# Kernel optimization log

Hardware: AMD Instinct MI355X
Metric: run time of the kernel (lower is better)

Reference implementation:

```python
import jax, jax.numpy as jnp
import numpy as np

N_SAMPLES, N_TIME, N_FEAT = 64, 4, 64
N_ENTITIES = 10000
D = N_TIME * N_FEAT  # 256
K = 10


def setup_inputs() -> dict:
    key = jax.random.key(0)
    k1, k2 = jax.random.split(key)
    query = jax.random.uniform(k1, (N_SAMPLES, N_TIME, N_FEAT), dtype=jnp.float32)
    # module state: self.enity_info, flattened view must be [n_entities, D]
    enity_info = jax.random.uniform(k2, (N_ENTITIES, D), dtype=jnp.float32)
    return {"query": query, "enity_info": enity_info, "k": K}


def reference(query, enity_info, k):
    n_samples = query.shape[0]
    q = query.reshape(n_samples, -1)                 # [n, d]
    e = enity_info.reshape(enity_info.shape[0], -1)  # [m, d]
    # pairwise Jaccard: sum(min) / sum(max) over feature dim
    inter = jnp.sum(jnp.minimum(q[:, None, :], e[None, :, :]), axis=2)  # [n, m]
    union = jnp.sum(jnp.maximum(q[:, None, :], e[None, :, :]), axis=2)  # [n, m]
    jaccard = inter / union                                             # [n, m]
    # torch.topk largest=True, sorted=True -> lax.top_k (descending)
    _, top_idx = jax.lax.top_k(jaccard, k)
    # torch.topk largest=False, sorted=True -> ascending smallest: top_k of negated
    _, bot_idx = jax.lax.top_k(-jaccard, k)
    return top_idx, bot_idx
```

## Files before the change

kernel.cpp:

```cpp
#include <hip/hip_runtime.h>
#include <math.h>
#include <limits.h>

#define NQ     64
#define NE     10000
#define K      10
#define NBLK   500
#define EPB    20
#define TPB    256
#define NWAVE  4
#define EPW    5
#define SLOT   11
#define SCALE  8388608.0f

__device__ __forceinline__ bool better_top(double v, int i, double v2, int i2) {
    return (v > v2) || (v == v2 && i < i2);
}

__device__ __forceinline__ void merge_slots16(double* Mv, unsigned short* Mi, int A, int B) {
    double ov[K]; unsigned short oi[K];
    int a = 0, b = 0;
#pragma unroll
    for (int o = 0; o < K; ++o) {
        double va = Mv[A * SLOT + a]; int ia = Mi[A * SLOT + a];
        double vb = Mv[B * SLOT + b]; int ib = Mi[B * SLOT + b];
        bool pick = better_top(va, ia, vb, ib);
        ov[o] = pick ? va : vb;
        oi[o] = (unsigned short)(pick ? ia : ib);
        if (pick) ++a; else ++b;
    }
#pragma unroll
    for (int o = 0; o < K; ++o) { Mv[A * SLOT + o] = ov[o]; Mi[A * SLOT + o] = oi[o]; }
}

#define CSWAP(v, ii, A, B)                                                 \
    {                                                                      \
        bool c_ = better_top(v[B], ii[B], v[A], ii[A]);                    \
        double tv_ = c_ ? v[B] : v[A]; double uv_ = c_ ? v[A] : v[B];      \
        int    ti_ = c_ ? ii[B] : ii[A]; int ui_ = c_ ? ii[A] : ii[B];     \
        v[A] = tv_; v[B] = uv_; ii[A] = ti_; ii[B] = ui_;                  \
    }
#define SORT5(v, ii)            \
    CSWAP(v, ii, 0, 1) CSWAP(v, ii, 3, 4) CSWAP(v, ii, 2, 4) \
    CSWAP(v, ii, 2, 3) CSWAP(v, ii, 0, 3) CSWAP(v, ii, 0, 2) \
    CSWAP(v, ii, 1, 4) CSWAP(v, ii, 1, 3) CSWAP(v, ii, 1, 2)

__global__ __launch_bounds__(256) void ent_sums(const float* __restrict__ E,
                                                unsigned* __restrict__ Se) {
    const int w = threadIdx.x >> 6, l = threadIdx.x & 63;
    const int j = blockIdx.x * 4 + w;
    float4 v = reinterpret_cast<const float4*>(E)[(size_t)j * 64 + l];
    unsigned s = (unsigned)(v.x * SCALE) + (unsigned)(v.y * SCALE)
               + (unsigned)(v.z * SCALE) + (unsigned)(v.w * SCALE);
#pragma unroll
    for (int m = 1; m < 64; m <<= 1) s += (unsigned)__shfl_xor((int)s, m, 64);
    if (l == 0) Se[j] = s;
}

__global__ __launch_bounds__(TPB, 2) void jac_part(
        const float* __restrict__ Q, const float* __restrict__ E,
        const unsigned* __restrict__ Se,
        double* __restrict__ pvT, double* __restrict__ pvB,
        int* __restrict__ piT, int* __restrict__ piB) {
    __shared__ uint4 QT[64 * 65];

    const int t = threadIdx.x;
    const int l = t & 63;
    const int w = t >> 6;
    const int b = blockIdx.x;
    const int ebase = b * EPB + w * EPW;

    const float4* E4 = (const float4*)E;
    const float4* Q4 = (const float4*)Q;

    float4 er[EPW];
#pragma unroll
    for (int s = 0; s < EPW; ++s) er[s] = E4[(size_t)(ebase + s) * 64 + l];
    unsigned se[EPW];
#pragma unroll
    for (int s = 0; s < EPW; ++s) se[s] = Se[ebase + s];

#pragma unroll
    for (int it = 0; it < 16; ++it) {
        const int f = t + TPB * it;
        float4 v = Q4[f];
        uint4 u;
        u.x = (unsigned)(v.x * SCALE); u.y = (unsigned)(v.y * SCALE);
        u.z = (unsigned)(v.z * SCALE); u.w = (unsigned)(v.w * SCALE);
        QT[(f & 63) * 65 + (f >> 6)] = u;
    }

    uint4 eu[EPW];
#pragma unroll
    for (int s = 0; s < EPW; ++s) {
        eu[s].x = (unsigned)(er[s].x * SCALE); eu[s].y = (unsigned)(er[s].y * SCALE);
        eu[s].z = (unsigned)(er[s].z * SCALE); eu[s].w = (unsigned)(er[s].w * SCALE);
    }
    __syncthreads();

    unsigned a0[EPW], a1[EPW];
#pragma unroll
    for (int s = 0; s < EPW; ++s) { a0[s] = 0; a1[s] = 0; }
    unsigned sq = 0;

#pragma unroll 8
    for (int g = 0; g < 64; ++g) {
        uint4 qv = QT[g * 65 + l];
        sq += (qv.x + qv.y) + (qv.z + qv.w);
#pragma unroll
        for (int s = 0; s < EPW; ++s) {
            unsigned ex = (unsigned)__builtin_amdgcn_readlane((int)eu[s].x, g);
            unsigned ey = (unsigned)__builtin_amdgcn_readlane((int)eu[s].y, g);
            unsigned ez = (unsigned)__builtin_amdgcn_readlane((int)eu[s].z, g);
            unsigned ew = (unsigned)__builtin_amdgcn_readlane((int)eu[s].w, g);
            a0[s] += min(qv.x, ex) + min(qv.y, ey);
            a1[s] += min(qv.z, ez) + min(qv.w, ew);
        }
    }

    double av[EPW]; int ai[EPW]; double bv[EPW]; int bi[EPW];
#pragma unroll
    for (int s = 0; s < EPW; ++s) {
        unsigned inter = a0[s] + a1[s];
        unsigned uni   = sq + se[s] - inter;
        double jac = (double)inter / (double)uni;
        av[s] = jac;  ai[s] = ebase + s;
        bv[s] = -jac; bi[s] = ebase + s;
    }
    SORT5(av, ai)
    SORT5(bv, bi)

    __syncthreads();
    double*         MvA = (double*)&QT[0];
    unsigned short* MiA = (unsigned short*)((char*)&QT[0] + 22528);
    double*         MvB = (double*)((char*)&QT[0] + 28160);
    unsigned short* MiB = (unsigned short*)((char*)&QT[0] + 50688);
    const int slot = w * 64 + l;

#pragma unroll
    for (int o = 0; o < EPW; ++o) {
        MvA[slot * SLOT + o] = av[o]; MiA[slot * SLOT + o] = (unsigned short)ai[o];
        MvB[slot * SLOT + o] = bv[o]; MiB[slot * SLOT + o] = (unsigned short)bi[o];
    }
#pragma unroll
    for (int o = EPW; o < K; ++o) {
        MvA[slot * SLOT + o] = -INFINITY; MiA[slot * SLOT + o] = 0xFFFFu;
        MvB[slot * SLOT + o] = -INFINITY; MiB[slot * SLOT + o] = 0xFFFFu;
    }
    __syncthreads();

    if (w < 2) {
        merge_slots16(MvA, MiA, w * 64 + l, (w + 2) * 64 + l);
        merge_slots16(MvB, MiB, w * 64 + l, (w + 2) * 64 + l);
    }
    __syncthreads();
    if (w == 0) {
        merge_slots16(MvA, MiA, l, 64 + l);
        merge_slots16(MvB, MiB, l, 64 + l);
        const size_t off = ((size_t)l * NBLK + b) * K;
#pragma unroll
        for (int o = 0; o < K; ++o) {
            pvT[off + o] = MvA[l * SLOT + o]; piT[off + o] = (int)MiA[l * SLOT + o];
            pvB[off + o] = MvB[l * SLOT + o]; piB[off + o] = (int)MiB[l * SLOT + o];
        }
    }
}

__global__ __launch_bounds__(256) void final_extract(
        const double* __restrict__ pvT, const double* __restrict__ pvB,
        const int* __restrict__ piT, const int* __restrict__ piB,
        int* __restrict__ out) {
    __shared__ double Lv[256 * K];
    __shared__ int    Li[256 * K];
    __shared__ double Wv[4];
    __shared__ int    Wi[4], Wo[4];
    __shared__ int    res[K];

    const int bid = blockIdx.x;
    const int q   = bid >> 1;
    const bool top = (bid & 1) == 0;
    const int t   = threadIdx.x;
    const int l   = t & 63;
    const int w   = t >> 6;

    const double* V = (top ? pvT : pvB) + (size_t)q * NBLK * K;
    const int*    I = (top ? piT : piB) + (size_t)q * NBLK * K;

    {
        double ov[K]; int oi[K];
        const int lb = t + 256;
        if (lb < NBLK) {
            int a = 0, bn = 0;
            const size_t sa = (size_t)t * K, sb = (size_t)lb * K;
#pragma unroll
            for (int o = 0; o < K; ++o) {
                double va = V[sa + a];  int ia = I[sa + a];
                double vb = V[sb + bn]; int ib = I[sb + bn];
                bool pick = better_top(va, ia, vb, ib);
                ov[o] = pick ? va : vb; oi[o] = pick ? ia : ib;
                if (pick) ++a; else ++bn;
            }
        } else {
#pragma unroll
            for (int o = 0; o < K; ++o) { ov[o] = V[(size_t)t * K + o]; oi[o] = I[(size_t)t * K + o]; }
        }
#pragma unroll
        for (int o = 0; o < K; ++o) { Lv[t * K + o] = ov[o]; Li[t * K + o] = oi[o]; }
    }
    __syncthreads();

    int h = 0;
    double hv = Lv[t * K];
    int    hi = Li[t * K];

    for (int r = 0; r < K; ++r) {
        double v = hv; int idx = hi; int own = t;
#pragma unroll
        for (int m = 1; m < 64; m <<= 1) {
            double ov = __shfl_xor(v, m, 64);
            int    oi = __shfl_xor(idx, m, 64);
            int    oo = __shfl_xor(own, m, 64);
            if (better_top(ov, oi, v, idx)) { v = ov; idx = oi; own = oo; }
        }
        if (l == 0) { Wv[w] = v; Wi[w] = idx; Wo[w] = own; }
        __syncthreads();
        double gv = Wv[0]; int gi = Wi[0], go = Wo[0];
#pragma unroll
        for (int ww = 1; ww < 4; ++ww)
            if (better_top(Wv[ww], Wi[ww], gv, gi)) { gv = Wv[ww]; gi = Wi[ww]; go = Wo[ww]; }
        if (t == go) {
            ++h;
            bool ok = h < K;
            hv = ok ? Lv[t * K + h] : -INFINITY;
            hi = ok ? Li[t * K + h] : INT_MAX;
        }
        if (t == 0) res[r] = gi;
        __syncthreads();
    }

    if (t < K) out[(top ? 0 : NQ * K) + q * K + t] = res[t];
}

extern "C" void kernel_launch(void* const* d_in, const int* in_sizes, int n_in,
                              void* d_out, int out_size, void* d_ws, size_t ws_size,
                              hipStream_t stream) {
    const float* Q = (const float*)d_in[0];
    const float* E = (const float*)d_in[1];
    int* out = (int*)d_out;

    char* ws = (char*)d_ws;
    unsigned* Se  = (unsigned*)(ws);
    double*   pvT = (double*)(ws + 40960);
    double*   pvB = (double*)(ws + 2600960);
    int*      piT = (int*)   (ws + 5160960);
    int*      piB = (int*)   (ws + 6440960);

    hipLaunchKernelGGL(ent_sums, dim3(NE / 4), dim3(256), 0, stream, E, Se);
    hipLaunchKernelGGL(jac_part, dim3(NBLK), dim3(TPB), 0, stream,
                       Q, E, Se, pvT, pvB, piT, piB);
    hipLaunchKernelGGL(final_extract, dim3(NQ * 2), dim3(256), 0, stream,
                       pvT, pvB, piT, piB, out);
}
```

Measured before the change: 53.33 us.

## Use 512-thread blocks with two entities per wave and 16-bit partial indices

```diff
diff --git a/kernel.cpp b/kernel.cpp
--- a/kernel.cpp
+++ b/kernel.cpp
@@ -5,11 +5,10 @@
 #define NQ     64
 #define NE     10000
 #define K      10
-#define NBLK   500
-#define EPB    20
-#define TPB    256
-#define NWAVE  4
-#define EPW    5
+#define NBLK   625
+#define EPB    16
+#define TPB    512
+#define EPW    2
 #define SLOT   11
 #define SCALE  8388608.0f
 
@@ -33,6 +32,25 @@
     for (int o = 0; o < K; ++o) { Mv[A * SLOT + o] = ov[o]; Mi[A * SLOT + o] = oi[o]; }
 }
 
+__device__ __forceinline__ void merge_lds_global(double* Lv, int* Li, int slot,
+                                                 const double* __restrict__ V,
+                                                 const unsigned short* __restrict__ I,
+                                                 int src) {
+    double ov[K]; int oi[K];
+    int a = 0, b = 0;
+#pragma unroll
+    for (int o = 0; o < K; ++o) {
+        double va = Lv[slot * K + a]; int ia = Li[slot * K + a];
+        double vb = V[(size_t)src * K + b]; int ib = (int)I[(size_t)src * K + b];
+        bool pick = better_top(va, ia, vb, ib);
+        ov[o] = pick ? va : vb;
+        oi[o] = pick ? ia : ib;
+        if (pick) ++a; else ++b;
+    }
+#pragma unroll
+    for (int o = 0; o < K; ++o) { Lv[slot * K + o] = ov[o]; Li[slot * K + o] = oi[o]; }
+}
+
 #define CSWAP(v, ii, A, B)                                                 \
     {                                                                      \
         bool c_ = better_top(v[B], ii[B], v[A], ii[A]);                    \
@@ -40,10 +58,6 @@
         int    ti_ = c_ ? ii[B] : ii[A]; int ui_ = c_ ? ii[A] : ii[B];     \
         v[A] = tv_; v[B] = uv_; ii[A] = ti_; ii[B] = ui_;                  \
     }
-#define SORT5(v, ii)            \
-    CSWAP(v, ii, 0, 1) CSWAP(v, ii, 3, 4) CSWAP(v, ii, 2, 4) \
-    CSWAP(v, ii, 2, 3) CSWAP(v, ii, 0, 3) CSWAP(v, ii, 0, 2) \
-    CSWAP(v, ii, 1, 4) CSWAP(v, ii, 1, 3) CSWAP(v, ii, 1, 2)
 
 __global__ __launch_bounds__(256) void ent_sums(const float* __restrict__ E,
                                                 unsigned* __restrict__ Se) {
@@ -61,7 +75,7 @@
         const float* __restrict__ Q, const float* __restrict__ E,
         const unsigned* __restrict__ Se,
         double* __restrict__ pvT, double* __restrict__ pvB,
-        int* __restrict__ piT, int* __restrict__ piB) {
+        unsigned short* __restrict__ piT, unsigned short* __restrict__ piB) {
     __shared__ uint4 QT[64 * 65];
 
     const int t = threadIdx.x;
@@ -81,7 +95,7 @@
     for (int s = 0; s < EPW; ++s) se[s] = Se[ebase + s];
 
 #pragma unroll
-    for (int it = 0; it < 16; ++it) {
+    for (int it = 0; it < 8; ++it) {
         const int f = t + TPB * it;
         float4 v = Q4[f];
         uint4 u;
@@ -127,48 +141,49 @@
         av[s] = jac;  ai[s] = ebase + s;
         bv[s] = -jac; bi[s] = ebase + s;
     }
-    SORT5(av, ai)
-    SORT5(bv, bi)
-
-    __syncthreads();
-    double*         MvA = (double*)&QT[0];
-    unsigned short* MiA = (unsigned short*)((char*)&QT[0] + 22528);
-    double*         MvB = (double*)((char*)&QT[0] + 28160);
-    unsigned short* MiB = (unsigned short*)((char*)&QT[0] + 50688);
+    CSWAP(av, ai, 0, 1)
+    CSWAP(bv, bi, 0, 1)
+
+    __syncthreads();
+    double*         Mv = (double*)&QT[0];
+    unsigned short* Mi = (unsigned short*)((char*)&QT[0] + 45056);
     const int slot = w * 64 + l;
 
 #pragma unroll
-    for (int o = 0; o < EPW; ++o) {
-        MvA[slot * SLOT + o] = av[o]; MiA[slot * SLOT + o] = (unsigned short)ai[o];
-        MvB[slot * SLOT + o] = bv[o]; MiB[slot * SLOT + o] = (unsigned short)bi[o];
-    }
-#pragma unroll
-    for (int o = EPW; o < K; ++o) {
-        MvA[slot * SLOT + o] = -INFINITY; MiA[slot * SLOT + o] = 0xFFFFu;
-        MvB[slot * SLOT + o] = -INFINITY; MiB[slot * SLOT + o] = 0xFFFFu;
-    }
-    __syncthreads();
-
-    if (w < 2) {
-        merge_slots16(MvA, MiA, w * 64 + l, (w + 2) * 64 + l);
-        merge_slots16(MvB, MiB, w * 64 + l, (w + 2) * 64 + l);
-    }
-    __syncthreads();
+    for (int o = 0; o < EPW; ++o) { Mv[slot * SLOT + o] = av[o]; Mi[slot * SLOT + o] = (unsigned short)ai[o]; }
+#pragma unroll
+    for (int o = EPW; o < K; ++o) { Mv[slot * SLOT + o] = -INFINITY; Mi[slot * SLOT + o] = 0xFFFFu; }
+    __syncthreads();
+    for (int s = 4; s >= 1; s >>= 1) {
+        if (w < s) merge_slots16(Mv, Mi, w * 64 + l, (w + s) * 64 + l);
+        __syncthreads();
+    }
     if (w == 0) {
-        merge_slots16(MvA, MiA, l, 64 + l);
-        merge_slots16(MvB, MiB, l, 64 + l);
         const size_t off = ((size_t)l * NBLK + b) * K;
 #pragma unroll
-        for (int o = 0; o < K; ++o) {
-            pvT[off + o] = MvA[l * SLOT + o]; piT[off + o] = (int)MiA[l * SLOT + o];
-            pvB[off + o] = MvB[l * SLOT + o]; piB[off + o] = (int)MiB[l * SLOT + o];
-        }
+        for (int o = 0; o < K; ++o) { pvT[off + o] = Mv[l * SLOT + o]; piT[off + o] = Mi[l * SLOT + o]; }
+    }
+    __syncthreads();
+
+#pragma unroll
+    for (int o = 0; o < EPW; ++o) { Mv[slot * SLOT + o] = bv[o]; Mi[slot * SLOT + o] = (unsigned short)bi[o]; }
+#pragma unroll
+    for (int o = EPW; o < K; ++o) { Mv[slot * SLOT + o] = -INFINITY; Mi[slot * SLOT + o] = 0xFFFFu; }
+    __syncthreads();
+    for (int s = 4; s >= 1; s >>= 1) {
+        if (w < s) merge_slots16(Mv, Mi, w * 64 + l, (w + s) * 64 + l);
+        __syncthreads();
+    }
+    if (w == 0) {
+        const size_t off = ((size_t)l * NBLK + b) * K;
+#pragma unroll
+        for (int o = 0; o < K; ++o) { pvB[off + o] = Mv[l * SLOT + o]; piB[off + o] = Mi[l * SLOT + o]; }
     }
 }
 
 __global__ __launch_bounds__(256) void final_extract(
         const double* __restrict__ pvT, const double* __restrict__ pvB,
-        const int* __restrict__ piT, const int* __restrict__ piB,
+        const unsigned short* __restrict__ piT, const unsigned short* __restrict__ piB,
         int* __restrict__ out) {
     __shared__ double Lv[256 * K];
     __shared__ int    Li[256 * K];
@@ -183,30 +198,13 @@
     const int l   = t & 63;
     const int w   = t >> 6;
 
-    const double* V = (top ? pvT : pvB) + (size_t)q * NBLK * K;
-    const int*    I = (top ? piT : piB) + (size_t)q * NBLK * K;
-
-    {
-        double ov[K]; int oi[K];
-        const int lb = t + 256;
-        if (lb < NBLK) {
-            int a = 0, bn = 0;
-            const size_t sa = (size_t)t * K, sb = (size_t)lb * K;
-#pragma unroll
-            for (int o = 0; o < K; ++o) {
-                double va = V[sa + a];  int ia = I[sa + a];
-                double vb = V[sb + bn]; int ib = I[sb + bn];
-                bool pick = better_top(va, ia, vb, ib);
-                ov[o] = pick ? va : vb; oi[o] = pick ? ia : ib;
-                if (pick) ++a; else ++bn;
-            }
-        } else {
-#pragma unroll
-            for (int o = 0; o < K; ++o) { ov[o] = V[(size_t)t * K + o]; oi[o] = I[(size_t)t * K + o]; }
-        }
-#pragma unroll
-        for (int o = 0; o < K; ++o) { Lv[t * K + o] = ov[o]; Li[t * K + o] = oi[o]; }
-    }
+    const double*         V = (top ? pvT : pvB) + (size_t)q * NBLK * K;
+    const unsigned short* I = (top ? piT : piB) + (size_t)q * NBLK * K;
+
+#pragma unroll
+    for (int o = 0; o < K; ++o) { Lv[t * K + o] = V[(size_t)t * K + o]; Li[t * K + o] = (int)I[(size_t)t * K + o]; }
+    for (int src = t + 256; src < NBLK; src += 256)
+        merge_lds_global(Lv, Li, t, V, I, src);
     __syncthreads();
 
     int h = 0;
@@ -249,11 +247,11 @@
     int* out = (int*)d_out;
 
     char* ws = (char*)d_ws;
-    unsigned* Se  = (unsigned*)(ws);
-    double*   pvT = (double*)(ws + 40960);
-    double*   pvB = (double*)(ws + 2600960);
-    int*      piT = (int*)   (ws + 5160960);
-    int*      piB = (int*)   (ws + 6440960);
+    unsigned*       Se  = (unsigned*)(ws);
+    double*         pvT = (double*)(ws + 40960);
+    double*         pvB = (double*)(ws + 3240960);
+    unsigned short* piT = (unsigned short*)(ws + 6440960);
+    unsigned short* piB = (unsigned short*)(ws + 7240960);
 
     hipLaunchKernelGGL(ent_sums, dim3(NE / 4), dim3(256), 0, stream, E, Se);
     hipLaunchKernelGGL(jac_part, dim3(NBLK), dim3(TPB), 0, stream,
```

Measured after the change: 62.85 us. +17.9%, slower.
